# Performance work log

Measured on AMD Instinct MI355X. Metric: run time of the kernel, lower is better.

## Reference

```python
import jax, jax.numpy as jnp
import numpy as np

HEAD_SIZE = 128
NUM_EMBED = 1024
BLOCK_SIZE = 2048


def setup_inputs() -> dict:
    key = jax.random.key(0)
    kx, kk, kq, kv = jax.random.split(key, 4)
    x = jax.random.normal(kx, (4, BLOCK_SIZE, NUM_EMBED), dtype=jnp.float32)
    s = 1.0 / np.sqrt(NUM_EMBED)
    Wk = jax.random.normal(kk, (NUM_EMBED, HEAD_SIZE), dtype=jnp.float32) * s
    Wq = jax.random.normal(kq, (NUM_EMBED, HEAD_SIZE), dtype=jnp.float32) * s
    Wv = jax.random.normal(kv, (NUM_EMBED, HEAD_SIZE), dtype=jnp.float32) * s
    return {"x": x, "Wk": Wk, "Wq": Wq, "Wv": Wv}


def reference(x, Wk, Wq, Wv):
    # x: [B, T, C]; W*: [C, H]
    B, T, C = x.shape
    k = x @ Wk          # [B, T, H]
    q = x @ Wq          # [B, T, H]
    v = x @ Wv          # [B, T, H]
    scale = k.shape[-1] ** -0.5
    wei = jnp.einsum('bth,bsh->bts', q, k) * scale  # [B, T, T]
    causal = jnp.tril(jnp.ones((T, T), dtype=bool))
    wei = jnp.where(causal, wei, -jnp.inf)
    wei = jax.nn.softmax(wei, axis=-1)
    out = jnp.einsum('bts,bsh->bth', wei, v)        # [B, T, H]
    return out
```

## Files before the change

### kernel.cpp

```cpp
#include <hip/hip_runtime.h>
#include <hip/hip_bf16.h>
#include <math.h>

#define B_ 4
#define T_ 2048
#define C_ 1024
#define H_ 128
#define SCALE 0.088388347648318447f

typedef unsigned short u16;
typedef __bf16 bf16x8 __attribute__((ext_vector_type(8)));
typedef float  f32x4  __attribute__((ext_vector_type(4)));
typedef u16    u16x8  __attribute__((ext_vector_type(8)));
typedef u16    u16x4  __attribute__((ext_vector_type(4)));

#define PO_OFF  0u
#define ML_OFF  18874368u
#define WBT_OFF 19169280u
#define QB_OFF  19955712u
#define KB_OFF  22052864u
#define VT_OFF  24150016u

__device__ __forceinline__ u16 f2bf(float f) {
    __hip_bfloat16 h = __float2bfloat16(f);
    return __builtin_bit_cast(u16, h);
}
__device__ __forceinline__ float bf2f(u16 u) {
    unsigned v = (unsigned)u << 16;
    return __builtin_bit_cast(float, v);
}

__device__ __forceinline__ void load_lds16(const void* g, void* l) {
    __builtin_amdgcn_global_load_lds(
        (const __attribute__((address_space(1))) unsigned int*)g,
        (__attribute__((address_space(3))) unsigned int*)l, 16, 0, 0);
}

__global__ __launch_bounds__(256) void convert_w(const float* __restrict__ Wq,
                                                 const float* __restrict__ Wk,
                                                 const float* __restrict__ Wv,
                                                 u16* __restrict__ wbT) {
    const int id = blockIdx.x * 256 + threadIdx.x;
    const int s = id >> 17;
    const int r = id & 131071;
    const int k = r >> 7, n = r & 127;
    const float* W = (s == 0) ? Wq : (s == 1) ? Wk : Wv;
    float v = W[k * 128 + n];
    if (s == 0) v *= SCALE;
    wbT[(s << 17) + (n << 10) + k] = f2bf(v);
}

__global__ __launch_bounds__(256) void gemm_qkv(
    const float* __restrict__ x, const u16* __restrict__ wbT,
    u16* __restrict__ qb, u16* __restrict__ kb, u16* __restrict__ vT)
{
    __shared__ u16 xs[2][2048];
    __shared__ u16 ws[2][8192];

    const int tid = threadIdx.x;
    const int w = tid >> 6, lane = tid & 63, lg = lane >> 4, lr = lane & 15;
    const int wm = w >> 1, wn = w & 1;
    const int s = blockIdx.y;
    const int m0 = blockIdx.x * 32;
    const u16* wsrc = wbT + (s << 17);

    const int xrow = tid >> 3;
    const int xseg = tid & 7;
    const float* xbase = x + (size_t)(m0 + xrow) * C_ + xseg * 8;
    const unsigned xsw = ((unsigned)xrow & 7u) << 4;

    unsigned wro[4], wco[4];
#pragma unroll
    for (int i = 0; i < 4; ++i) {
        const unsigned o = (unsigned)(w * 4 + i) * 1024u + (unsigned)lane * 16u;
        const unsigned o2 = o ^ (((o >> 7) & 7u) << 4);
        wro[i] = o2 >> 7; wco[i] = (o2 & 127u) >> 1;
    }

    f32x4 acc[4] = {};

    {
        const float4 f0 = ((const float4*)xbase)[0], f1 = ((const float4*)xbase)[1];
#pragma unroll
        for (int i = 0; i < 4; ++i)
            load_lds16(wsrc + (size_t)wro[i] * C_ + wco[i], &ws[0][(w * 4 + i) * 512]);
        u16x8 pk;
        pk[0] = f2bf(f0.x); pk[1] = f2bf(f0.y); pk[2] = f2bf(f0.z); pk[3] = f2bf(f0.w);
        pk[4] = f2bf(f1.x); pk[5] = f2bf(f1.y); pk[6] = f2bf(f1.z); pk[7] = f2bf(f1.w);
        *(u16x8*)((char*)xs[0] + xrow * 128 + (((unsigned)xseg * 16) ^ xsw)) = pk;
    }
    __syncthreads();

    int buf = 0;
    for (int k0 = 0; k0 < C_; k0 += 64) {
        const bool pf = (k0 + 64 < C_);
        float4 g0, g1;
        if (pf) {
            const float* xn = xbase + k0 + 64;
            g0 = ((const float4*)xn)[0]; g1 = ((const float4*)xn)[1];
#pragma unroll
            for (int i = 0; i < 4; ++i)
                load_lds16(wsrc + (size_t)wro[i] * C_ + (k0 + 64) + wco[i],
                           &ws[buf ^ 1][(w * 4 + i) * 512]);
        }

        const int arow = wm * 16 + lr;
        const unsigned asw = ((unsigned)arow & 7u) << 4;
#pragma unroll
        for (int kc = 0; kc < 2; ++kc) {
            const unsigned kb_ = (unsigned)(kc * 64 + lg * 16);
            const bf16x8 af = *(const bf16x8*)((const char*)xs[buf] + arow * 128 + (kb_ ^ asw));
            bf16x8 bfr[4];
#pragma unroll
            for (int ni = 0; ni < 4; ++ni) {
                const int n = wn * 64 + ni * 16 + lr;
                bfr[ni] = *(const bf16x8*)((const char*)ws[buf] + n * 128 + (kb_ ^ (((unsigned)n & 7u) << 4)));
            }
#pragma unroll
            for (int ni = 0; ni < 4; ++ni)
                acc[ni] = __builtin_amdgcn_mfma_f32_16x16x32_bf16(af, bfr[ni], acc[ni], 0, 0, 0);
        }

        if (pf) {
            u16x8 pk;
            pk[0] = f2bf(g0.x); pk[1] = f2bf(g0.y); pk[2] = f2bf(g0.z); pk[3] = f2bf(g0.w);
            pk[4] = f2bf(g1.x); pk[5] = f2bf(g1.y); pk[6] = f2bf(g1.z); pk[7] = f2bf(g1.w);
            *(u16x8*)((char*)xs[buf ^ 1] + xrow * 128 + (((unsigned)xseg * 16) ^ xsw)) = pk;
        }
        __syncthreads();
        buf ^= 1;
    }

    if (s < 2) {
        u16* dst = (s == 0) ? qb : kb;
#pragma unroll
        for (int ni = 0; ni < 4; ++ni) {
            const int trow = m0 + wm * 16 + lg * 4;
            const int col = wn * 64 + ni * 16 + lr;
#pragma unroll
            for (int r = 0; r < 4; ++r)
                dst[(size_t)(trow + r) * H_ + col] = f2bf(acc[ni][r]);
        }
    } else {
#pragma unroll
        for (int ni = 0; ni < 4; ++ni) {
            const int trow = m0 + wm * 16 + lg * 4;
            const int bb = trow >> 11, t = trow & 2047;
            const int d = wn * 64 + ni * 16 + lr;
            u16x4 pk;
            pk[0] = f2bf(acc[ni][0]); pk[1] = f2bf(acc[ni][1]);
            pk[2] = f2bf(acc[ni][2]); pk[3] = f2bf(acc[ni][3]);
            *(u16x4*)&vT[((size_t)bb * 128 + d) * 2048 + t] = pk;
        }
    }
}

__global__ __launch_bounds__(256) void attn_split(
    const u16* __restrict__ qb, const u16* __restrict__ kb,
    const u16* __restrict__ vT, u16* __restrict__ po, float* __restrict__ ml)
{
    __shared__ u16 ks[2][4096];
    __shared__ u16 vs[2][128 * 36];

    const int jt = blockIdx.x, sp = blockIdx.y, b = blockIdx.z;
    const int kt0 = sp * 8;
    const int ktend_all = 2 * jt + 2;
    if (kt0 >= ktend_all) return;
    const int kt_end = min(kt0 + 8, ktend_all);

    const int tid = threadIdx.x;
    const int w = tid >> 6, lane = tid & 63, lg = lane >> 4, lr = lane & 15;
    const int qrow_base = jt * 64 + w * 16;

    const u16* kbB = kb + ((size_t)(b << 11)) * H_;
    const u16* vbB = vT + (size_t)b * 128 * 2048;

    unsigned krow[2], kcolb[2];
#pragma unroll
    for (int i = 0; i < 2; ++i) {
        const unsigned o_ = (unsigned)(w * 2 + i) * 1024u + (unsigned)lane * 16u;
        const unsigned o2 = o_ ^ (((o_ >> 8) & 7u) << 4);
        krow[i] = o2 >> 8; kcolb[i] = o2 & 255u;
    }
    int vd[2], vc[2];
#pragma unroll
    for (int i = 0; i < 2; ++i) {
        const int idx = i * 256 + tid;
        vd[i] = idx >> 2; vc[i] = idx & 3;
    }

    const u16* qp = qb + ((size_t)(b << 11) + qrow_base + lr) * H_;
    bf16x8 qf[4];
#pragma unroll
    for (int kc = 0; kc < 4; ++kc)
        qf[kc] = *(const bf16x8*)&qp[kc * 32 + lg * 8];

    u16x8 vr[2];
    {
        const u16* kbase = kbB + (size_t)kt0 * 32 * H_;
#pragma unroll
        for (int i = 0; i < 2; ++i)
            load_lds16((const char*)kbase + krow[i] * 256 + kcolb[i], &ks[0][(w * 2 + i) * 512]);
        const u16* vbase = vbB + (size_t)kt0 * 32;
#pragma unroll
        for (int i = 0; i < 2; ++i)
            vr[i] = *(const u16x8*)&vbase[(size_t)vd[i] * 2048 + vc[i] * 8];
#pragma unroll
        for (int i = 0; i < 2; ++i) {
            char* rb = (char*)vs[0] + vd[i] * 72 + (vc[i] & 2) * 4;
            *(u16x4*)(rb + ((2 * vc[i]) & 3) * 16)     = __builtin_shufflevector(vr[i], vr[i], 0, 1, 2, 3);
            *(u16x4*)(rb + ((2 * vc[i] + 1) & 3) * 16) = __builtin_shufflevector(vr[i], vr[i], 4, 5, 6, 7);
        }
    }
    __syncthreads();

    f32x4 o[8] = {};
    float m_run = -1e30f, l_run = 0.f;
    int cur = 0;

    for (int kt = kt0; kt < kt_end; ++kt) {
        const bool pf = (kt + 1 < kt_end);
        if (pf) {
            const u16* kbase = kbB + (size_t)(kt + 1) * 32 * H_;
#pragma unroll
            for (int i = 0; i < 2; ++i)
                load_lds16((const char*)kbase + krow[i] * 256 + kcolb[i],
                           &ks[cur ^ 1][(w * 2 + i) * 512]);
            const u16* vbase = vbB + (size_t)(kt + 1) * 32;
#pragma unroll
            for (int i = 0; i < 2; ++i)
                vr[i] = *(const u16x8*)&vbase[(size_t)vd[i] * 2048 + vc[i] * 8];
        }

        f32x4 s0 = {0.f, 0.f, 0.f, 0.f}, s1 = {0.f, 0.f, 0.f, 0.f};
        const unsigned swz = ((unsigned)lr & 7u) << 4;
#pragma unroll
        for (int kc = 0; kc < 4; ++kc) {
            const unsigned byte = ((unsigned)(kc * 64 + lg * 16)) ^ swz;
            const bf16x8 kf0 = *(const bf16x8*)((const char*)ks[cur] + lr * 256 + byte);
            const bf16x8 kf1 = *(const bf16x8*)((const char*)ks[cur] + lr * 256 + 4096 + byte);
            s0 = __builtin_amdgcn_mfma_f32_16x16x32_bf16(kf0, qf[kc], s0, 0, 0, 0);
            s1 = __builtin_amdgcn_mfma_f32_16x16x32_bf16(kf1, qf[kc], s1, 0, 0, 0);
        }

        if (kt * 32 + 31 > qrow_base) {
            const int qg = qrow_base + lr;
            const int kvb = kt * 32 + lg * 4;
#pragma unroll
            for (int r = 0; r < 4; ++r) {
                if (kvb + r > qg)      s0[r] = -INFINITY;
                if (kvb + 16 + r > qg) s1[r] = -INFINITY;
            }
        }

        float mt = fmaxf(fmaxf(fmaxf(s0[0], s0[1]), fmaxf(s0[2], s0[3])),
                         fmaxf(fmaxf(s1[0], s1[1]), fmaxf(s1[2], s1[3])));
        mt = fmaxf(mt, __shfl_xor(mt, 16));
        mt = fmaxf(mt, __shfl_xor(mt, 32));
        if (__any(mt > m_run + 8.f)) {
            const float mn = fmaxf(m_run, mt);
            const float f = __expf(m_run - mn);
            const float fb0 = __shfl(f, lg * 4 + 0);
            const float fb1 = __shfl(f, lg * 4 + 1);
            const float fb2 = __shfl(f, lg * 4 + 2);
            const float fb3 = __shfl(f, lg * 4 + 3);
#pragma unroll
            for (int ni = 0; ni < 8; ++ni) {
                o[ni][0] *= fb0; o[ni][1] *= fb1; o[ni][2] *= fb2; o[ni][3] *= fb3;
            }
            l_run *= f;
            m_run = mn;
        }
        const float p0 = __expf(s0[0] - m_run), p1 = __expf(s0[1] - m_run);
        const float p2 = __expf(s0[2] - m_run), p3 = __expf(s0[3] - m_run);
        const float p4 = __expf(s1[0] - m_run), p5 = __expf(s1[1] - m_run);
        const float p6 = __expf(s1[2] - m_run), p7 = __expf(s1[3] - m_run);
        float sum = ((p0 + p1) + (p2 + p3)) + ((p4 + p5) + (p6 + p7));
        sum += __shfl_xor(sum, 16);
        sum += __shfl_xor(sum, 32);
        l_run += sum;

        bf16x8 pa;
        pa[0] = (__bf16)p0; pa[1] = (__bf16)p1; pa[2] = (__bf16)p2; pa[3] = (__bf16)p3;
        pa[4] = (__bf16)p4; pa[5] = (__bf16)p5; pa[6] = (__bf16)p6; pa[7] = (__bf16)p7;

#pragma unroll
        for (int ni = 0; ni < 8; ++ni) {
            const bf16x8 vf = *(const bf16x8*)((const char*)vs[cur] + (ni * 16 + lr) * 72 + lg * 16);
            o[ni] = __builtin_amdgcn_mfma_f32_16x16x32_bf16(pa, vf, o[ni], 0, 0, 0);
        }

        if (pf) {
#pragma unroll
            for (int i = 0; i < 2; ++i) {
                char* rb = (char*)vs[cur ^ 1] + vd[i] * 72 + (vc[i] & 2) * 4;
                *(u16x4*)(rb + ((2 * vc[i]) & 3) * 16)     = __builtin_shufflevector(vr[i], vr[i], 0, 1, 2, 3);
                *(u16x4*)(rb + ((2 * vc[i] + 1) & 3) * 16) = __builtin_shufflevector(vr[i], vr[i], 4, 5, 6, 7);
            }
        }
        __syncthreads();
        cur ^= 1;
    }

    const int a = jt >> 2, b3 = jt & 3;
    const int slot = (a + 1) * (2 * a + b3) + sp;
    u16* pob = po + (size_t)(b * 144 + slot) * 64 * 128;
#pragma unroll
    for (int ni = 0; ni < 8; ++ni) {
        const int col = ni * 16 + lr;
#pragma unroll
        for (int rj = 0; rj < 4; ++rj)
            pob[(w * 16 + lg * 4 + rj) * 128 + col] = f2bf(o[ni][rj]);
    }
    if (lg == 0) {
        float* mlb = ml + (size_t)(b * 144 + slot) * 128;
        mlb[w * 16 + lr] = m_run;
        mlb[64 + w * 16 + lr] = l_run;
    }
}

__global__ __launch_bounds__(256) void attn_combine(
    const u16* __restrict__ po, const float* __restrict__ ml,
    float* __restrict__ out)
{
    const int rid = (blockIdx.x << 3) + (threadIdx.x >> 5);
    const int b = blockIdx.y;
    const int d4 = (threadIdx.x & 31) * 4;
    const int jt = rid >> 6, row = rid & 63;
    const int a = jt >> 2, b3 = jt & 3;
    const int slot0 = (a + 1) * (2 * a + b3);
    const int c = a + 1;

    float M = -INFINITY;
#pragma unroll
    for (int si = 0; si < 8; ++si)
        if (si < c) M = fmaxf(M, ml[(size_t)(b * 144 + slot0 + si) * 128 + row]);

    float L = 0.f;
    float a0 = 0.f, a1 = 0.f, a2 = 0.f, a3 = 0.f;
#pragma unroll
    for (int si = 0; si < 8; ++si) {
        if (si < c) {
            const float* mlb = ml + (size_t)(b * 144 + slot0 + si) * 128;
            const float wgt = __expf(mlb[row] - M);
            L += wgt * mlb[64 + row];
            const u16x4 t = *(const u16x4*)&po[((size_t)(b * 144 + slot0 + si) * 64 + row) * 128 + d4];
            a0 = fmaf(wgt, bf2f(t[0]), a0); a1 = fmaf(wgt, bf2f(t[1]), a1);
            a2 = fmaf(wgt, bf2f(t[2]), a2); a3 = fmaf(wgt, bf2f(t[3]), a3);
        }
    }
    const float inv = 1.f / L;
    *(float4*)&out[((size_t)(b << 11) + rid) * H_ + d4] =
        make_float4(a0 * inv, a1 * inv, a2 * inv, a3 * inv);
}

extern "C" void kernel_launch(void* const* d_in, const int* in_sizes, int n_in,
                              void* d_out, int out_size, void* d_ws, size_t ws_size,
                              hipStream_t stream) {
    const float* x  = (const float*)d_in[0];
    const float* Wk = (const float*)d_in[1];
    const float* Wq = (const float*)d_in[2];
    const float* Wv = (const float*)d_in[3];
    float* out = (float*)d_out;

    u16* po   = (u16*)((char*)d_ws + PO_OFF);
    float* ml = (float*)((char*)d_ws + ML_OFF);
    u16* wbT  = (u16*)((char*)d_ws + WBT_OFF);
    u16* qb   = (u16*)((char*)d_ws + QB_OFF);
    u16* kb   = (u16*)((char*)d_ws + KB_OFF);
    u16* vT   = (u16*)((char*)d_ws + VT_OFF);

    convert_w<<<1536, 256, 0, stream>>>(Wq, Wk, Wv, wbT);
    gemm_qkv<<<dim3(256, 3), 256, 0, stream>>>(x, wbT, qb, kb, vT);
    attn_split<<<dim3(32, 8, 4), 256, 0, stream>>>(qb, kb, vT, po, ml);
    attn_combine<<<dim3(256, 4), 256, 0, stream>>>(po, ml, out);
}
```

Measured before the change: 63.81 us.

## Double KV tile size to 64 rows per iteration in split attention

Each attention loop iteration now processes a 64-key tile instead of 32, doubling the LDS K/V buffers. Each split still covers 256 keys, now as 4 iterations instead of 8. This halves the number of barriers, softmax rescale checks and shuffle reductions per key. In exchange it uses more LDS per block, which may reduce occupancy, and more registers for the larger score tile. The causal-mask granularity becomes coarser, so more masked work is done on diagonal tiles.

```diff
diff --git a/kernel.cpp b/kernel.cpp
--- a/kernel.cpp
+++ b/kernel.cpp
@@ -159,14 +159,14 @@
     const u16* __restrict__ qb, const u16* __restrict__ kb,
     const u16* __restrict__ vT, u16* __restrict__ po, float* __restrict__ ml)
 {
-    __shared__ u16 ks[2][4096];
-    __shared__ u16 vs[2][128 * 36];
+    __shared__ u16 ks[2][8192];
+    __shared__ u16 vs[2][9216];
 
     const int jt = blockIdx.x, sp = blockIdx.y, b = blockIdx.z;
-    const int kt0 = sp * 8;
-    const int ktend_all = 2 * jt + 2;
-    if (kt0 >= ktend_all) return;
-    const int kt_end = min(kt0 + 8, ktend_all);
+    const int nt_all = jt + 1;
+    const int kt0 = sp * 4;
+    if (kt0 >= nt_all) return;
+    const int kt_end = min(kt0 + 4, nt_all);
 
     const int tid = threadIdx.x;
     const int w = tid >> 6, lane = tid & 63, lg = lane >> 4, lr = lane & 15;
@@ -175,10 +175,10 @@
     const u16* kbB = kb + ((size_t)(b << 11)) * H_;
     const u16* vbB = vT + (size_t)b * 128 * 2048;
 
-    unsigned krow[2], kcolb[2];
-#pragma unroll
-    for (int i = 0; i < 2; ++i) {
-        const unsigned o_ = (unsigned)(w * 2 + i) * 1024u + (unsigned)lane * 16u;
+    unsigned krow[4], kcolb[4];
+#pragma unroll
+    for (int i = 0; i < 4; ++i) {
+        const unsigned o_ = (unsigned)(w * 4 + i) * 1024u + (unsigned)lane * 16u;
         const unsigned o2 = o_ ^ (((o_ >> 8) & 7u) << 4);
         krow[i] = o2 >> 8; kcolb[i] = o2 & 255u;
     }
@@ -195,22 +195,26 @@
     for (int kc = 0; kc < 4; ++kc)
         qf[kc] = *(const bf16x8*)&qp[kc * 32 + lg * 8];
 
-    u16x8 vr[2];
+    u16x8 vr[4];
     {
-        const u16* kbase = kbB + (size_t)kt0 * 32 * H_;
-#pragma unroll
-        for (int i = 0; i < 2; ++i)
-            load_lds16((const char*)kbase + krow[i] * 256 + kcolb[i], &ks[0][(w * 2 + i) * 512]);
-        const u16* vbase = vbB + (size_t)kt0 * 32;
-#pragma unroll
-        for (int i = 0; i < 2; ++i)
-            vr[i] = *(const u16x8*)&vbase[(size_t)vd[i] * 2048 + vc[i] * 8];
-#pragma unroll
-        for (int i = 0; i < 2; ++i) {
-            char* rb = (char*)vs[0] + vd[i] * 72 + (vc[i] & 2) * 4;
-            *(u16x4*)(rb + ((2 * vc[i]) & 3) * 16)     = __builtin_shufflevector(vr[i], vr[i], 0, 1, 2, 3);
-            *(u16x4*)(rb + ((2 * vc[i] + 1) & 3) * 16) = __builtin_shufflevector(vr[i], vr[i], 4, 5, 6, 7);
-        }
+        const u16* kbase = kbB + (size_t)kt0 * 64 * H_;
+#pragma unroll
+        for (int i = 0; i < 4; ++i)
+            load_lds16((const char*)kbase + krow[i] * 256 + kcolb[i], &ks[0][(w * 4 + i) * 512]);
+        const u16* vbase = vbB + (size_t)kt0 * 64;
+#pragma unroll
+        for (int h = 0; h < 2; ++h)
+#pragma unroll
+            for (int i = 0; i < 2; ++i)
+                vr[h * 2 + i] = *(const u16x8*)&vbase[(size_t)vd[i] * 2048 + h * 32 + vc[i] * 8];
+#pragma unroll
+        for (int h = 0; h < 2; ++h)
+#pragma unroll
+            for (int i = 0; i < 2; ++i) {
+                char* rb = (char*)vs[0] + h * 9216 + vd[i] * 72 + (vc[i] & 2) * 4;
+                *(u16x4*)(rb + ((2 * vc[i]) & 3) * 16)     = __builtin_shufflevector(vr[h * 2 + i], vr[h * 2 + i], 0, 1, 2, 3);
+                *(u16x4*)(rb + ((2 * vc[i] + 1) & 3) * 16) = __builtin_shufflevector(vr[h * 2 + i], vr[h * 2 + i], 4, 5, 6, 7);
+            }
     }
     __syncthreads();
 
@@ -221,40 +225,46 @@
     for (int kt = kt0; kt < kt_end; ++kt) {
         const bool pf = (kt + 1 < kt_end);
         if (pf) {
-            const u16* kbase = kbB + (size_t)(kt + 1) * 32 * H_;
-#pragma unroll
-            for (int i = 0; i < 2; ++i)
+            const u16* kbase = kbB + (size_t)(kt + 1) * 64 * H_;
+#pragma unroll
+            for (int i = 0; i < 4; ++i)
                 load_lds16((const char*)kbase + krow[i] * 256 + kcolb[i],
-                           &ks[cur ^ 1][(w * 2 + i) * 512]);
-            const u16* vbase = vbB + (size_t)(kt + 1) * 32;
-#pragma unroll
-            for (int i = 0; i < 2; ++i)
-                vr[i] = *(const u16x8*)&vbase[(size_t)vd[i] * 2048 + vc[i] * 8];
-        }
-
-        f32x4 s0 = {0.f, 0.f, 0.f, 0.f}, s1 = {0.f, 0.f, 0.f, 0.f};
+                           &ks[cur ^ 1][(w * 4 + i) * 512]);
+            const u16* vbase = vbB + (size_t)(kt + 1) * 64;
+#pragma unroll
+            for (int h = 0; h < 2; ++h)
+#pragma unroll
+                for (int i = 0; i < 2; ++i)
+                    vr[h * 2 + i] = *(const u16x8*)&vbase[(size_t)vd[i] * 2048 + h * 32 + vc[i] * 8];
+        }
+
+        f32x4 sS[4] = {};
         const unsigned swz = ((unsigned)lr & 7u) << 4;
 #pragma unroll
         for (int kc = 0; kc < 4; ++kc) {
             const unsigned byte = ((unsigned)(kc * 64 + lg * 16)) ^ swz;
-            const bf16x8 kf0 = *(const bf16x8*)((const char*)ks[cur] + lr * 256 + byte);
-            const bf16x8 kf1 = *(const bf16x8*)((const char*)ks[cur] + lr * 256 + 4096 + byte);
-            s0 = __builtin_amdgcn_mfma_f32_16x16x32_bf16(kf0, qf[kc], s0, 0, 0, 0);
-            s1 = __builtin_amdgcn_mfma_f32_16x16x32_bf16(kf1, qf[kc], s1, 0, 0, 0);
-        }
-
-        if (kt * 32 + 31 > qrow_base) {
+#pragma unroll
+            for (int si = 0; si < 4; ++si) {
+                const bf16x8 kf = *(const bf16x8*)((const char*)ks[cur] + si * 4096 + lr * 256 + byte);
+                sS[si] = __builtin_amdgcn_mfma_f32_16x16x32_bf16(kf, qf[kc], sS[si], 0, 0, 0);
+            }
+        }
+
+        if (kt * 64 + 63 > qrow_base) {
             const int qg = qrow_base + lr;
-            const int kvb = kt * 32 + lg * 4;
-#pragma unroll
-            for (int r = 0; r < 4; ++r) {
-                if (kvb + r > qg)      s0[r] = -INFINITY;
-                if (kvb + 16 + r > qg) s1[r] = -INFINITY;
-            }
-        }
-
-        float mt = fmaxf(fmaxf(fmaxf(s0[0], s0[1]), fmaxf(s0[2], s0[3])),
-                         fmaxf(fmaxf(s1[0], s1[1]), fmaxf(s1[2], s1[3])));
+#pragma unroll
+            for (int si = 0; si < 4; ++si) {
+                const int kvb = kt * 64 + si * 16 + lg * 4;
+#pragma unroll
+                for (int r = 0; r < 4; ++r)
+                    if (kvb + r > qg) sS[si][r] = -INFINITY;
+            }
+        }
+
+        float mt = fmaxf(fmaxf(fmaxf(sS[0][0], sS[0][1]), fmaxf(sS[0][2], sS[0][3])),
+                         fmaxf(fmaxf(sS[1][0], sS[1][1]), fmaxf(sS[1][2], sS[1][3])));
+        mt = fmaxf(mt, fmaxf(fmaxf(fmaxf(sS[2][0], sS[2][1]), fmaxf(sS[2][2], sS[2][3])),
+                             fmaxf(fmaxf(sS[3][0], sS[3][1]), fmaxf(sS[3][2], sS[3][3]))));
         mt = fmaxf(mt, __shfl_xor(mt, 16));
         mt = fmaxf(mt, __shfl_xor(mt, 32));
         if (__any(mt > m_run + 8.f)) {
@@ -271,32 +281,42 @@
             l_run *= f;
             m_run = mn;
         }
-        const float p0 = __expf(s0[0] - m_run), p1 = __expf(s0[1] - m_run);
-        const float p2 = __expf(s0[2] - m_run), p3 = __expf(s0[3] - m_run);
-        const float p4 = __expf(s1[0] - m_run), p5 = __expf(s1[1] - m_run);
-        const float p6 = __expf(s1[2] - m_run), p7 = __expf(s1[3] - m_run);
-        float sum = ((p0 + p1) + (p2 + p3)) + ((p4 + p5) + (p6 + p7));
+        float p[16];
+#pragma unroll
+        for (int si = 0; si < 4; ++si)
+#pragma unroll
+            for (int r = 0; r < 4; ++r)
+                p[si * 4 + r] = __expf(sS[si][r] - m_run);
+        float sum = ((p[0] + p[1]) + (p[2] + p[3])) + ((p[4] + p[5]) + (p[6] + p[7]))
+                  + ((p[8] + p[9]) + (p[10] + p[11])) + ((p[12] + p[13]) + (p[14] + p[15]));
         sum += __shfl_xor(sum, 16);
         sum += __shfl_xor(sum, 32);
         l_run += sum;
 
-        bf16x8 pa;
-        pa[0] = (__bf16)p0; pa[1] = (__bf16)p1; pa[2] = (__bf16)p2; pa[3] = (__bf16)p3;
-        pa[4] = (__bf16)p4; pa[5] = (__bf16)p5; pa[6] = (__bf16)p6; pa[7] = (__bf16)p7;
+        bf16x8 pa0, pa1;
+#pragma unroll
+        for (int r = 0; r < 4; ++r) {
+            pa0[r] = (__bf16)p[r];      pa0[4 + r] = (__bf16)p[4 + r];
+            pa1[r] = (__bf16)p[8 + r];  pa1[4 + r] = (__bf16)p[12 + r];
+        }
 
 #pragma unroll
         for (int ni = 0; ni < 8; ++ni) {
-            const bf16x8 vf = *(const bf16x8*)((const char*)vs[cur] + (ni * 16 + lr) * 72 + lg * 16);
-            o[ni] = __builtin_amdgcn_mfma_f32_16x16x32_bf16(pa, vf, o[ni], 0, 0, 0);
+            const bf16x8 vf0 = *(const bf16x8*)((const char*)vs[cur] + (ni * 16 + lr) * 72 + lg * 16);
+            const bf16x8 vf1 = *(const bf16x8*)((const char*)vs[cur] + 9216 + (ni * 16 + lr) * 72 + lg * 16);
+            o[ni] = __builtin_amdgcn_mfma_f32_16x16x32_bf16(pa0, vf0, o[ni], 0, 0, 0);
+            o[ni] = __builtin_amdgcn_mfma_f32_16x16x32_bf16(pa1, vf1, o[ni], 0, 0, 0);
         }
 
         if (pf) {
 #pragma unroll
-            for (int i = 0; i < 2; ++i) {
-                char* rb = (char*)vs[cur ^ 1] + vd[i] * 72 + (vc[i] & 2) * 4;
-                *(u16x4*)(rb + ((2 * vc[i]) & 3) * 16)     = __builtin_shufflevector(vr[i], vr[i], 0, 1, 2, 3);
-                *(u16x4*)(rb + ((2 * vc[i] + 1) & 3) * 16) = __builtin_shufflevector(vr[i], vr[i], 4, 5, 6, 7);
-            }
+            for (int h = 0; h < 2; ++h)
+#pragma unroll
+                for (int i = 0; i < 2; ++i) {
+                    char* rb = (char*)vs[cur ^ 1] + h * 9216 + vd[i] * 72 + (vc[i] & 2) * 4;
+                    *(u16x4*)(rb + ((2 * vc[i]) & 3) * 16)     = __builtin_shufflevector(vr[h * 2 + i], vr[h * 2 + i], 0, 1, 2, 3);
+                    *(u16x4*)(rb + ((2 * vc[i] + 1) & 3) * 16) = __builtin_shufflevector(vr[h * 2 + i], vr[h * 2 + i], 4, 5, 6, 7);
+                }
         }
         __syncthreads();
         cur ^= 1;
```

Result: faster. 59.21 us, median of 2 (-7.2%).
